# Optimization experiments

Hardware: AMD Instinct MI355X
Metric: run time of the kernel (lower is better)

## Reference

```python
import jax, jax.numpy as jnp
import numpy as np

N, E, D, H, O, L = 50000, 400000, 128, 128, 64, 2


def setup_inputs() -> dict:
    key = jax.random.key(0)
    ks = jax.random.split(key, 24)
    s = 0.05
    rn = lambda k, shape: jax.random.normal(k, shape, jnp.float32) * s
    # random edges with no self-loops (dst = src + nonzero offset mod N)
    src = jax.random.randint(ks[0], (E,), 0, N, dtype=jnp.int32)
    off = jax.random.randint(ks[1], (E,), 1, N, dtype=jnp.int32)
    dst = (src + off) % N
    edge_index = jnp.stack([src, dst])  # [2, E] int32
    return {
        "x": rn(ks[2], (N, D)),
        "edge_index": edge_index,
        "attn_W": rn(ks[3], (L, 2 * D, 2)),
        "attn_b": rn(ks[4], (L, 2)),
        "mlp_W1": rn(ks[5], (L, D, H)),
        "mlp_b1": rn(ks[6], (L, H)),
        "mlp_W2": rn(ks[7], (L, H, H)),
        "mlp_b2": rn(ks[8], (L, H)),
        "bn_gamma": jnp.ones((L, H), jnp.float32),   # torch BatchNorm1d default affine init
        "bn_beta": jnp.zeros((L, H), jnp.float32),
        "gru_Wih": rn(ks[9], (D, 3 * H)),
        "gru_Whh": rn(ks[10], (H, 3 * H)),
        "gru_bih": rn(ks[11], (3 * H,)),
        "gru_bhh": rn(ks[12], (3 * H,)),
        "last_W1": rn(ks[13], (H, H)),
        "last_b1": rn(ks[14], (H,)),
        "last_W2": rn(ks[15], (H, O)),
        "last_b2": rn(ks[16], (O,)),
    }


def reference(x, edge_index, attn_W, attn_b, mlp_W1, mlp_b1, mlp_W2, mlp_b2,
              bn_gamma, bn_beta, gru_Wih, gru_Whh, gru_bih, gru_bhh,
              last_W1, last_b1, last_W2, last_b2):
    n = x.shape[0]
    # symmetrize edge list: message (nbr -> node) for both directions
    node = jnp.concatenate([edge_index[0], edge_index[1]])  # destination
    nbr = jnp.concatenate([edge_index[1], edge_index[0]])   # source / neighbor
    deg = jax.ops.segment_sum(jnp.ones((node.shape[0], 1), x.dtype), node, num_segments=n)
    has_nbr = deg > 0

    h_state = jnp.zeros((n, gru_Whh.shape[0]), x.dtype)
    for l in range(attn_W.shape[0]):
        feats = x[nbr]  # [2E, d] gather
        s_agg = jax.ops.segment_sum(feats, node, num_segments=n)
        m_agg = jax.ops.segment_max(feats, node, num_segments=n)
        m_agg = jnp.where(has_nbr, m_agg, jnp.zeros_like(m_agg))  # isolated nodes stay 0
        # attention over {sum, max} aggregations
        scores = jnp.concatenate([s_agg, m_agg], axis=1) @ attn_W[l] + attn_b[l]  # [n, 2]
        w = jax.nn.softmax(scores, axis=1)
        comb = x + w[:, :1] * s_agg + w[:, 1:] * m_agg
        # MLP (in -> hidden, ReLU, hidden -> out)
        z = jax.nn.relu(comb @ mlp_W1[l] + mlp_b1[l]) @ mlp_W2[l] + mlp_b2[l]
        # BatchNorm1d in eval mode with running stats (mean 0, var 1): affine only
        z = z * bn_gamma[l] + bn_beta[l]
        # GRUCell
        gi = z @ gru_Wih + gru_bih
        gh = h_state @ gru_Whh + gru_bhh
        ir, iz, inn = jnp.split(gi, 3, axis=1)
        hr, hz, hn = jnp.split(gh, 3, axis=1)
        r = jax.nn.sigmoid(ir + hr)
        u = jax.nn.sigmoid(iz + hz)
        ncand = jnp.tanh(inn + r * hn)
        h_state = (1.0 - u) * ncand + u * h_state
        x = h_state
    # final node-level MLP
    out = jax.nn.relu(x @ last_W1 + last_b1) @ last_W2 + last_b2
    return out
```

## Files before the change

### kernel.cpp

```cpp
#include <hip/hip_runtime.h>
#include <math.h>

typedef unsigned short u16;
typedef __attribute__((ext_vector_type(8))) short bf16x8;
typedef __attribute__((ext_vector_type(4))) float f32x4;

#define ADJ_CAP 96

__device__ __forceinline__ u16 f2b(float f) {
    union { float f; unsigned u; } v; v.f = f;
    unsigned r = (v.u + 0x7FFF + ((v.u >> 16) & 1)) >> 16;
    return (u16)r;
}
__device__ __forceinline__ float b2f(u16 h) {
    union { unsigned u; float f; } v; v.u = (unsigned)h << 16;
    return v.f;
}
__device__ __forceinline__ float fsig(float x) { return 1.f / (1.f + __expf(-x)); }
__device__ __forceinline__ float ftanh(float x) {
    float e = __expf(2.f * x);
    return 1.f - 2.f / (e + 1.f);
}

__device__ __forceinline__ void gll16(const void* g, void* l) {
    __builtin_amdgcn_global_load_lds(
        (const __attribute__((address_space(1))) void*)g,
        (__attribute__((address_space(3))) void*)l, 16, 0, 0);
}

__device__ __forceinline__ void conv_chunk(const float* __restrict__ src,
                                           u16* __restrict__ dst, int c, int NC) {
    int sl = c / NC, n = c - sl * NC;
    u16 tmp[8];
#pragma unroll
    for (int i = 0; i < 8; ++i) tmp[i] = f2b(src[(size_t)(sl * 8 + i) * NC + n]);
    *(uint4*)(dst + (size_t)c * 8) = *(const uint4*)tmp;
}

__global__ void k_pro(const int* __restrict__ ei, int* __restrict__ cnt,
                      u16* __restrict__ adj, int E, int N,
                      const float* __restrict__ W1, const float* __restrict__ W2,
                      const float* __restrict__ Wih, const float* __restrict__ Whh,
                      const float* __restrict__ lW1, const float* __restrict__ lW2,
                      u16* __restrict__ tW1, u16* __restrict__ tW2,
                      u16* __restrict__ tGRU,
                      u16* __restrict__ tlW1, u16* __restrict__ tlW2, int L,
                      const float* __restrict__ x, u16* __restrict__ xb, int n8) {
    const int EB = (E + 255) >> 8;
    const int nwc = L * 4096 + 12288 + 3072;
    const int WB = (nwc + 255) >> 8;
    int b = blockIdx.x;
    if (b < EB * 8) {
        const int part = b & 7, chunk = b >> 3;
        const int span = (N + 7) >> 3;
        const int nlo = part * span;
        const int nhi = (nlo + span < N) ? nlo + span : N;
        int e = chunk * 256 + threadIdx.x;
        if (e < E) {
            int s = ei[e], d = ei[E + e];
            if (s >= nlo && s < nhi) {
                int p = atomicAdd(&cnt[s], 1);
                adj[(size_t)s * ADJ_CAP + p] = (u16)d;
            }
            if (d >= nlo && d < nhi) {
                int q = atomicAdd(&cnt[d], 1);
                adj[(size_t)d * ADJ_CAP + q] = (u16)s;
            }
        }
        return;
    }
    b -= EB * 8;
    if (b < WB) {
        int c = b * 256 + threadIdx.x;
        if (c >= nwc) return;
        if (c < L * 2048) { int l = c >> 11; conv_chunk(W1 + (size_t)l * 16384, tW1 + (size_t)l * 16384, c & 2047, 128); return; }
        c -= L * 2048;
        if (c < L * 2048) { int l = c >> 11; conv_chunk(W2 + (size_t)l * 16384, tW2 + (size_t)l * 16384, c & 2047, 128); return; }
        c -= L * 2048;
        if (c < 12288) {
            int s = c >> 9, r = c & 511;
            int q = r >> 7, mat = (r >> 6) & 1, cc = r & 63;
            int h = s / 12, s2 = s % 12, kc = s2 / 3, g = s2 % 3;
            int ocol = g * 128 + h * 64 + cc;
            const float* src = mat ? Whh : Wih;
            int kb = (kc * 4 + q) * 8;
            u16 tmp[8];
#pragma unroll
            for (int e = 0; e < 8; ++e) tmp[e] = f2b(src[(size_t)(kb + e) * 384 + ocol]);
            *(uint4*)(tGRU + (size_t)c * 8) = *(const uint4*)tmp;
            return;
        }
        c -= 12288;
        if (c < 2048) { conv_chunk(lW1, tlW1, c, 128); return; }
        c -= 2048;
        if (c < 1024) { conv_chunk(lW2, tlW2, c, 64); return; }
        return;
    }
    b -= WB;
    {
        int i = b * 256 + threadIdx.x;
        if (i < n8) {
            float4 a = *(const float4*)(x + (size_t)i * 8);
            float4 bb = *(const float4*)(x + (size_t)i * 8 + 4);
            u16 t[8] = {f2b(a.x), f2b(a.y), f2b(a.z), f2b(a.w),
                        f2b(bb.x), f2b(bb.y), f2b(bb.z), f2b(bb.w)};
            *(uint4*)(xb + (size_t)i * 8) = *(const uint4*)t;
        }
    }
}

__global__ __launch_bounds__(256) void k_agg(const u16* __restrict__ xb,
                                             const u16* __restrict__ adj,
                                             const int* __restrict__ cnt,
                                             const float* __restrict__ aW,
                                             const float* __restrict__ ab,
                                             u16* __restrict__ comb, int N) {
    int n = blockIdx.x * 4 + (threadIdx.x >> 6);
    if (n >= N) return;
    int l = threadIdx.x & 63;
    int half = l >> 5, e0 = (l & 31) * 4;
    int beg = n * ADJ_CAP;
    int deg = cnt[n];
    int end = beg + deg;
    float s0 = 0.f, s1 = 0.f, s2 = 0.f, s3 = 0.f;
    float m0 = -3.402823e38f, m1 = m0, m2 = m0, m3 = m0;
    int j = beg + half;
    for (; j + 14 < end; j += 16) {
        ushort4 v[8];
#pragma unroll
        for (int u = 0; u < 8; ++u) {
            int a = adj[j + 2 * u];
            v[u] = *(const ushort4*)(xb + (size_t)a * 128 + e0);
        }
#pragma unroll
        for (int u = 0; u < 8; ++u) {
            float f0 = b2f(v[u].x), f1 = b2f(v[u].y), f2 = b2f(v[u].z), f3 = b2f(v[u].w);
            s0 += f0; s1 += f1; s2 += f2; s3 += f3;
            m0 = fmaxf(m0, f0); m1 = fmaxf(m1, f1);
            m2 = fmaxf(m2, f2); m3 = fmaxf(m3, f3);
        }
    }
    for (; j < end; j += 2) {
        int nb = adj[j];
        ushort4 v = *(const ushort4*)(xb + (size_t)nb * 128 + e0);
        float f0 = b2f(v.x), f1 = b2f(v.y), f2 = b2f(v.z), f3 = b2f(v.w);
        s0 += f0; s1 += f1; s2 += f2; s3 += f3;
        m0 = fmaxf(m0, f0); m1 = fmaxf(m1, f1); m2 = fmaxf(m2, f2); m3 = fmaxf(m3, f3);
    }
    s0 += __shfl_xor(s0, 32); m0 = fmaxf(m0, __shfl_xor(m0, 32));
    s1 += __shfl_xor(s1, 32); m1 = fmaxf(m1, __shfl_xor(m1, 32));
    s2 += __shfl_xor(s2, 32); m2 = fmaxf(m2, __shfl_xor(m2, 32));
    s3 += __shfl_xor(s3, 32); m3 = fmaxf(m3, __shfl_xor(m3, 32));
    if (deg == 0) { m0 = m1 = m2 = m3 = 0.f; }
    float p0 = 0.f, p1 = 0.f;
    {
        float2 w0v = *(const float2*)(aW + (size_t)e0 * 2);
        float2 w1v = *(const float2*)(aW + (size_t)(e0 + 1) * 2);
        float2 w2v = *(const float2*)(aW + (size_t)(e0 + 2) * 2);
        float2 w3v = *(const float2*)(aW + (size_t)(e0 + 3) * 2);
        float2 u0v = *(const float2*)(aW + (size_t)(128 + e0) * 2);
        float2 u1v = *(const float2*)(aW + (size_t)(128 + e0 + 1) * 2);
        float2 u2v = *(const float2*)(aW + (size_t)(128 + e0 + 2) * 2);
        float2 u3v = *(const float2*)(aW + (size_t)(128 + e0 + 3) * 2);
        p0 = s0 * w0v.x + s1 * w1v.x + s2 * w2v.x + s3 * w3v.x
           + m0 * u0v.x + m1 * u1v.x + m2 * u2v.x + m3 * u3v.x;
        p1 = s0 * w0v.y + s1 * w1v.y + s2 * w2v.y + s3 * w3v.y
           + m0 * u0v.y + m1 * u1v.y + m2 * u2v.y + m3 * u3v.y;
    }
#pragma unroll
    for (int o = 16; o; o >>= 1) { p0 += __shfl_xor(p0, o); p1 += __shfl_xor(p1, o); }
    p0 += ab[0]; p1 += ab[1];
    float pm = fmaxf(p0, p1);
    float ea = __expf(p0 - pm), eb = __expf(p1 - pm);
    float w0 = ea / (ea + eb), w1 = 1.f - w0;
    if (half == 0) {
        ushort4 xv = *(const ushort4*)(xb + (size_t)n * 128 + e0);
        ushort4 o;
        o.x = f2b(b2f(xv.x) + w0 * s0 + w1 * m0);
        o.y = f2b(b2f(xv.y) + w0 * s1 + w1 * m1);
        o.z = f2b(b2f(xv.z) + w0 * s2 + w1 * m2);
        o.w = f2b(b2f(xv.w) + w0 * s3 + w1 * m3);
        *(ushort4*)(comb + (size_t)n * 128 + e0) = o;
    }
}

template <bool H0, bool WF32>
__global__ __launch_bounds__(256, 4) void k_layer(
    const u16* __restrict__ Cb, const u16* __restrict__ Hb,
    const float* __restrict__ Hf,
    const u16* __restrict__ W1t, const float* __restrict__ b1,
    const u16* __restrict__ W2t, const float* __restrict__ b2,
    const float* __restrict__ gam, const float* __restrict__ bet,
    const u16* __restrict__ tG,
    const float* __restrict__ bih, const float* __restrict__ bhh,
    float* __restrict__ HnF, u16* __restrict__ HnB, int M) {
    __shared__ __align__(16) u16 x_s[64 * 16 * 8];
    __shared__ __align__(16) u16 b_s[3][4096];
    const int t = threadIdx.x;
    const int m0 = blockIdx.x * 64;
    const int wid = t >> 6, lane = t & 63, lo = lane & 15, hi = lane >> 4;
    const int arow = 16 * wid + lo;

    auto issue = [&](int s) {
        const u16* g = (s < 4) ? (W1t + (size_t)s * 4096)
                     : (s < 8) ? (W2t + (size_t)(s - 4) * 4096)
                               : (tG + (size_t)(s - 8) * 4096);
        char* l = (char*)b_s[s % 3] + wid * 2048;
        const char* gp = (const char*)g + wid * 2048 + lane * 16;
        gll16(gp, l);
        gll16(gp + 1024, l + 1024);
    };

    float b1r[8], g2r[8], t2r[8];
#pragma unroll
    for (int j = 0; j < 8; ++j) {
        int c = 16 * j + lo;
        b1r[j] = b1[c];
        float gv = gam[c];
        g2r[j] = gv;
        t2r[j] = b2[c] * gv + bet[c];
    }
#pragma unroll
    for (int i = 0; i < 4; ++i) {
        int off = (i * 4 + wid) * 1024;
        int row = (off >> 8) + (lane >> 4);
        int sl = lane & 15;
        int gr = m0 + row; gr = gr < M ? gr : M - 1;
        gll16(Cb + (size_t)gr * 128 + ((sl ^ (row & 7)) * 8), (char*)x_s + off);
    }
    issue(0);
    issue(1);

    f32x4 acc[8];
#pragma unroll
    for (int j = 0; j < 8; ++j) acc[j] = (f32x4)0.f;

#pragma unroll
    for (int ks = 0; ks < 4; ++ks) {
        const int p = ks;
        asm volatile("s_waitcnt vmcnt(2)" ::: "memory");
        __builtin_amdgcn_s_barrier();
        issue(p + 2);
        bf16x8 af = *(const bf16x8*)&x_s[(arow * 16 + ((ks * 4 + hi) ^ (arow & 7))) * 8];
        const u16* buf = b_s[p % 3];
        __builtin_amdgcn_s_setprio(1);
#pragma unroll
        for (int j = 0; j < 8; ++j) {
            bf16x8 bf = *(const bf16x8*)&buf[((size_t)hi * 128 + 16 * j + lo) * 8];
            acc[j] = __builtin_amdgcn_mfma_f32_16x16x32_bf16(af, bf, acc[j], 0, 0, 0);
        }
        __builtin_amdgcn_s_setprio(0);
    }
#pragma unroll
    for (int j = 0; j < 8; ++j) {
        int c = 16 * j + lo;
#pragma unroll
        for (int q = 0; q < 4; ++q) {
            int row = 16 * wid + hi * 4 + q;
            float v = fmaxf(acc[j][q] + b1r[j], 0.f);
            int sl = c >> 3;
            x_s[(row * 16 + (sl ^ (row & 7))) * 8 + (c & 7)] = f2b(v);
        }
        acc[j] = (f32x4)0.f;
    }

#pragma unroll
    for (int ks = 0; ks < 4; ++ks) {
        const int p = 4 + ks;
        asm volatile("s_waitcnt vmcnt(2)" ::: "memory");
        __builtin_amdgcn_s_barrier();
        issue(p + 2);
        bf16x8 af = *(const bf16x8*)&x_s[(arow * 16 + ((ks * 4 + hi) ^ (arow & 7))) * 8];
        const u16* buf = b_s[p % 3];
        __builtin_amdgcn_s_setprio(1);
#pragma unroll
        for (int j = 0; j < 8; ++j) {
            bf16x8 bf = *(const bf16x8*)&buf[((size_t)hi * 128 + 16 * j + lo) * 8];
            acc[j] = __builtin_amdgcn_mfma_f32_16x16x32_bf16(af, bf, acc[j], 0, 0, 0);
        }
        __builtin_amdgcn_s_setprio(0);
    }
#pragma unroll
    for (int j = 0; j < 8; ++j) {
        int c = 16 * j + lo;
#pragma unroll
        for (int q = 0; q < 4; ++q) {
            int row = 16 * wid + hi * 4 + q;
            float v = acc[j][q] * g2r[j] + t2r[j];
            int sl = c >> 3;
            x_s[(row * 16 + (sl ^ (row & 7))) * 8 + (c & 7)] = f2b(v);
        }
    }
    bf16x8 hreg[4];
    if (!H0) {
        int gr = m0 + arow; gr = gr < M ? gr : M - 1;
#pragma unroll
        for (int kc = 0; kc < 4; ++kc)
            hreg[kc] = *(const bf16x8*)(Hb + (size_t)gr * 128 + (kc * 4 + hi) * 8);
    }

    f32x4 racc[4], uacc[4], nza[4], nha[4];

    auto epi = [&](int h) {
#pragma unroll
        for (int ct = 0; ct < 4; ++ct) {
            int c = h * 64 + ct * 16 + lo;
            float b_r = bih[c] + bhh[c];
            float b_u = bih[c + 128] + bhh[c + 128];
            float b_in = bih[c + 256], b_hn = bhh[c + 256];
#pragma unroll
            for (int q = 0; q < 4; ++q) {
                int r = m0 + 16 * wid + hi * 4 + q;
                if (r < M) {
                    float rr = fsig(racc[ct][q] + b_r);
                    float uu = fsig(uacc[ct][q] + b_u);
                    float hterm = H0 ? b_hn : (nha[ct][q] + b_hn);
                    float nn = ftanh(nza[ct][q] + b_in + rr * hterm);
                    float hv = H0 ? 0.f : Hf[(size_t)r * 128 + c];
                    float o = (1.f - uu) * nn + uu * hv;
                    if (WF32) HnF[(size_t)r * 128 + c] = o;
                    HnB[(size_t)r * 128 + c] = f2b(o);
                }
            }
        }
    };

#pragma unroll
    for (int h = 0; h < 2; ++h) {
#pragma unroll
        for (int j = 0; j < 4; ++j) {
            racc[j] = (f32x4)0.f; uacc[j] = (f32x4)0.f;
            nza[j] = (f32x4)0.f; nha[j] = (f32x4)0.f;
        }
#pragma unroll
        for (int kc = 0; kc < 4; ++kc) {
            bf16x8 zf;
#pragma unroll
            for (int g = 0; g < 3; ++g) {
                const int p = 8 + h * 12 + kc * 3 + g;
                if (p == 31) asm volatile("s_waitcnt vmcnt(0)" ::: "memory");
                else         asm volatile("s_waitcnt vmcnt(2)" ::: "memory");
                __builtin_amdgcn_s_barrier();
                if (p + 2 <= 31) issue(p + 2);
                if (g == 0)
                    zf = *(const bf16x8*)&x_s[(arow * 16 + ((kc * 4 + hi) ^ (arow & 7))) * 8];
                const u16* buf = b_s[p % 3];
                __builtin_amdgcn_s_setprio(1);
#pragma unroll
                for (int jj = 0; jj < 4; ++jj) {
                    bf16x8 wi = *(const bf16x8*)&buf[((size_t)hi * 128 + jj * 16 + lo) * 8];
                    if (g == 0)      racc[jj] = __builtin_amdgcn_mfma_f32_16x16x32_bf16(zf, wi, racc[jj], 0, 0, 0);
                    else if (g == 1) uacc[jj] = __builtin_amdgcn_mfma_f32_16x16x32_bf16(zf, wi, uacc[jj], 0, 0, 0);
                    else             nza[jj]  = __builtin_amdgcn_mfma_f32_16x16x32_bf16(zf, wi, nza[jj], 0, 0, 0);
                    if (!H0) {
                        bf16x8 wh = *(const bf16x8*)&buf[((size_t)hi * 128 + 64 + jj * 16 + lo) * 8];
                        if (g == 0)      racc[jj] = __builtin_amdgcn_mfma_f32_16x16x32_bf16(hreg[kc], wh, racc[jj], 0, 0, 0);
                        else if (g == 1) uacc[jj] = __builtin_amdgcn_mfma_f32_16x16x32_bf16(hreg[kc], wh, uacc[jj], 0, 0, 0);
                        else             nha[jj]  = __builtin_amdgcn_mfma_f32_16x16x32_bf16(hreg[kc], wh, nha[jj], 0, 0, 0);
                    }
                }
                __builtin_amdgcn_s_setprio(0);
            }
        }
        epi(h);
    }
}

__global__ __launch_bounds__(256, 2) void k_final(const u16* __restrict__ Hb,
                                                  const u16* __restrict__ W1t,
                                                  const float* __restrict__ b1,
                                                  const u16* __restrict__ W2t,
                                                  const float* __restrict__ b2,
                                                  float* __restrict__ out, int M) {
    __shared__ __align__(16) u16 x_s[64 * 16 * 8];
    __shared__ __align__(16) u16 w_s[16 * 128 * 8];
    const int t = threadIdx.x;
    const int m0 = blockIdx.x * 64;
    const int w = t >> 6, l = t & 63, lo = l & 15, hi = l >> 4;
    const int arow = 16 * w + lo;
#pragma unroll
    for (int i = 0; i < 4; ++i) {
        int idx = t + i * 256;
        int row = idx >> 4, sl = idx & 15;
        int gr = m0 + row; gr = gr < M ? gr : M - 1;
        *(uint4*)&x_s[(row * 16 + (sl ^ (row & 7))) * 8] =
            *(const uint4*)(Hb + (size_t)gr * 128 + sl * 8);
    }
#pragma unroll
    for (int i = 0; i < 8; ++i) {
        int idx = t + i * 256;
        *(uint4*)&w_s[idx * 8] = *(const uint4*)(W1t + (size_t)idx * 8);
    }
    __syncthreads();
    f32x4 acc[8];
#pragma unroll
    for (int j = 0; j < 8; ++j) acc[j] = (f32x4)0.f;
#pragma unroll
    for (int ks = 0; ks < 4; ++ks) {
        bf16x8 af = *(const bf16x8*)&x_s[(arow * 16 + ((ks * 4 + hi) ^ (arow & 7))) * 8];
#pragma unroll
        for (int j = 0; j < 8; ++j) {
            bf16x8 bf = *(const bf16x8*)&w_s[((ks * 4 + hi) * 128 + 16 * j + lo) * 8];
            acc[j] = __builtin_amdgcn_mfma_f32_16x16x32_bf16(af, bf, acc[j], 0, 0, 0);
        }
    }
    __syncthreads();
#pragma unroll
    for (int j = 0; j < 8; ++j) {
        int c = 16 * j + lo;
        float bv = b1[c];
#pragma unroll
        for (int q = 0; q < 4; ++q) {
            int row = 16 * w + hi * 4 + q;
            float v = fmaxf(acc[j][q] + bv, 0.f);
            int sl = c >> 3;
            x_s[(row * 16 + (sl ^ (row & 7))) * 8 + (c & 7)] = f2b(v);
        }
    }
#pragma unroll
    for (int i = 0; i < 4; ++i) {
        int idx = t + i * 256;
        *(uint4*)&w_s[idx * 8] = *(const uint4*)(W2t + (size_t)idx * 8);
    }
    __syncthreads();
    f32x4 a2[4];
#pragma unroll
    for (int j = 0; j < 4; ++j) a2[j] = (f32x4)0.f;
#pragma unroll
    for (int ks = 0; ks < 4; ++ks) {
        bf16x8 af = *(const bf16x8*)&x_s[(arow * 16 + ((ks * 4 + hi) ^ (arow & 7))) * 8];
#pragma unroll
        for (int j = 0; j < 4; ++j) {
            bf16x8 bf = *(const bf16x8*)&w_s[((ks * 4 + hi) * 64 + 16 * j + lo) * 8];
            a2[j] = __builtin_amdgcn_mfma_f32_16x16x32_bf16(af, bf, a2[j], 0, 0, 0);
        }
    }
#pragma unroll
    for (int j = 0; j < 4; ++j) {
        int c = 16 * j + lo;
        float bv = b2[c];
#pragma unroll
        for (int q = 0; q < 4; ++q) {
            int r = m0 + 16 * w + hi * 4 + q;
            if (r < M) out[(size_t)r * 64 + c] = a2[j][q] + bv;
        }
    }
}

extern "C" void kernel_launch(void* const* d_in, const int* in_sizes, int n_in,
                              void* d_out, int out_size, void* d_ws, size_t ws_size,
                              hipStream_t stream) {
    const float* x   = (const float*)d_in[0];
    const int*   ei  = (const int*)d_in[1];
    const float* aW  = (const float*)d_in[2];
    const float* ab  = (const float*)d_in[3];
    const float* W1  = (const float*)d_in[4];
    const float* b1  = (const float*)d_in[5];
    const float* W2  = (const float*)d_in[6];
    const float* b2  = (const float*)d_in[7];
    const float* gam = (const float*)d_in[8];
    const float* bet = (const float*)d_in[9];
    const float* Wih = (const float*)d_in[10];
    const float* Whh = (const float*)d_in[11];
    const float* bih = (const float*)d_in[12];
    const float* bhh = (const float*)d_in[13];
    const float* lW1 = (const float*)d_in[14];
    const float* lb1 = (const float*)d_in[15];
    const float* lW2 = (const float*)d_in[16];
    const float* lb2 = (const float*)d_in[17];

    const int N = in_sizes[0] / 128;
    const int E = in_sizes[1] / 2;
    const int L = in_sizes[3] / 2;
    float* out = (float*)d_out;

    char* ws = (char*)d_ws;
    size_t off = 0;
    auto alloc = [&](size_t bytes) -> void* {
        void* p = ws + off;
        off = (off + bytes + 255) & ~(size_t)255;
        return p;
    };
    int* cnt  = (int*)alloc((size_t)N * 4);
    u16* adj  = (u16*)alloc((size_t)N * ADJ_CAP * 2);
    u16* tW1  = (u16*)alloc((size_t)L * 16384 * 2);
    u16* tW2  = (u16*)alloc((size_t)L * 16384 * 2);
    u16* tGRU = (u16*)alloc((size_t)98304 * 2);
    u16* tlW1 = (u16*)alloc((size_t)16384 * 2);
    u16* tlW2 = (u16*)alloc((size_t)8192 * 2);
    u16* xb   = (u16*)alloc((size_t)N * 128 * 2);
    u16* comb = (u16*)alloc((size_t)N * 128 * 2);
    float* hF = (float*)alloc((size_t)N * 128 * 4);
    u16* hAb  = (u16*)alloc((size_t)N * 128 * 2);
    u16* hBb  = (u16*)alloc((size_t)N * 128 * 2);
    (void)ws_size; (void)n_in; (void)out_size;

    hipMemsetAsync(cnt, 0, (size_t)N * 4, stream);

    const int EB = (E + 255) / 256;
    const int nwc = L * 4096 + 12288 + 3072;
    const int WB = (nwc + 255) / 256;
    const int FB = (N * 16 + 255) / 256;
    k_pro<<<EB * 8 + WB + FB, 256, 0, stream>>>(ei, cnt, adj, E, N,
                                                W1, W2, Wih, Whh, lW1, lW2,
                                                tW1, tW2, tGRU, tlW1, tlW2, L,
                                                x, xb, N * 16);

    const int mb = (N + 63) / 64;
    k_agg<<<(N + 3) / 4, 256, 0, stream>>>(xb, adj, cnt, aW, ab, comb, N);
    k_layer<true, true><<<mb, 256, 0, stream>>>(
        comb, nullptr, nullptr, tW1, b1, tW2, b2, gam, bet,
        tGRU, bih, bhh, hF, hAb, N);
    k_agg<<<(N + 3) / 4, 256, 0, stream>>>(hAb, adj, cnt, aW + 512, ab + 2, comb, N);
    k_layer<false, false><<<mb, 256, 0, stream>>>(
        comb, hAb, hF, tW1 + 16384, b1 + 128, tW2 + 16384, b2 + 128,
        gam + 128, bet + 128, tGRU, bih, bhh, nullptr, hBb, N);

    k_final<<<(N + 63) / 64, 256, 0, stream>>>(hBb, tlW1, lb1, tlW2, lb2, out, N);
}
```

Before: 222.4 us.

## Fuse final MLP into last GRU layer, drop fp32 hidden state, widen agg loads

```diff
diff --git a/kernel.cpp b/kernel.cpp
--- a/kernel.cpp
+++ b/kernel.cpp
@@ -14,6 +14,10 @@
 }
 __device__ __forceinline__ float b2f(u16 h) {
     union { unsigned u; float f; } v; v.u = (unsigned)h << 16;
+    return v.f;
+}
+__device__ __forceinline__ float u2f(unsigned u) {
+    union { unsigned u; float f; } v; v.u = u;
     return v.f;
 }
 __device__ __forceinline__ float fsig(float x) { return 1.f / (1.f + __expf(-x)); }
@@ -118,93 +122,105 @@
     int n = blockIdx.x * 4 + (threadIdx.x >> 6);
     if (n >= N) return;
     int l = threadIdx.x & 63;
-    int half = l >> 5, e0 = (l & 31) * 4;
-    int beg = n * ADJ_CAP;
-    int deg = cnt[n];
-    int end = beg + deg;
-    float s0 = 0.f, s1 = 0.f, s2 = 0.f, s3 = 0.f;
-    float m0 = -3.402823e38f, m1 = m0, m2 = m0, m3 = m0;
-    int j = beg + half;
-    for (; j + 14 < end; j += 16) {
-        ushort4 v[8];
-#pragma unroll
-        for (int u = 0; u < 8; ++u) {
-            int a = adj[j + 2 * u];
-            v[u] = *(const ushort4*)(xb + (size_t)a * 128 + e0);
-        }
-#pragma unroll
-        for (int u = 0; u < 8; ++u) {
-            float f0 = b2f(v[u].x), f1 = b2f(v[u].y), f2 = b2f(v[u].z), f3 = b2f(v[u].w);
-            s0 += f0; s1 += f1; s2 += f2; s3 += f3;
-            m0 = fmaxf(m0, f0); m1 = fmaxf(m1, f1);
-            m2 = fmaxf(m2, f2); m3 = fmaxf(m3, f3);
-        }
-    }
-    for (; j < end; j += 2) {
-        int nb = adj[j];
-        ushort4 v = *(const ushort4*)(xb + (size_t)nb * 128 + e0);
-        float f0 = b2f(v.x), f1 = b2f(v.y), f2 = b2f(v.z), f3 = b2f(v.w);
-        s0 += f0; s1 += f1; s2 += f2; s3 += f3;
-        m0 = fmaxf(m0, f0); m1 = fmaxf(m1, f1); m2 = fmaxf(m2, f2); m3 = fmaxf(m3, f3);
-    }
-    s0 += __shfl_xor(s0, 32); m0 = fmaxf(m0, __shfl_xor(m0, 32));
-    s1 += __shfl_xor(s1, 32); m1 = fmaxf(m1, __shfl_xor(m1, 32));
-    s2 += __shfl_xor(s2, 32); m2 = fmaxf(m2, __shfl_xor(m2, 32));
-    s3 += __shfl_xor(s3, 32); m3 = fmaxf(m3, __shfl_xor(m3, 32));
-    if (deg == 0) { m0 = m1 = m2 = m3 = 0.f; }
+    int grp = l >> 4;
+    int f0 = (l & 15) * 8;
+    int beg = n * ADJ_CAP, deg = cnt[n], end = beg + deg;
+    float s[8], m[8];
+#pragma unroll
+    for (int i = 0; i < 8; ++i) { s[i] = 0.f; m[i] = -3.402823e38f; }
+
+    auto acc8 = [&](uint4 v) {
+        unsigned d[4] = {v.x, v.y, v.z, v.w};
+#pragma unroll
+        for (int i = 0; i < 4; ++i) {
+            float a0 = u2f(d[i] << 16);
+            float a1 = u2f(d[i] & 0xFFFF0000u);
+            s[2 * i] += a0;     m[2 * i] = fmaxf(m[2 * i], a0);
+            s[2 * i + 1] += a1; m[2 * i + 1] = fmaxf(m[2 * i + 1], a1);
+        }
+    };
+
+    int j = beg + grp;
+    for (; j + 4 < end; j += 8) {
+        int a0 = adj[j], a1 = adj[j + 4];
+        uint4 v0 = *(const uint4*)(xb + (size_t)a0 * 128 + f0);
+        uint4 v1 = *(const uint4*)(xb + (size_t)a1 * 128 + f0);
+        acc8(v0);
+        acc8(v1);
+    }
+    if (j < end) {
+        int a = adj[j];
+        uint4 v = *(const uint4*)(xb + (size_t)a * 128 + f0);
+        acc8(v);
+    }
+#pragma unroll
+    for (int i = 0; i < 8; ++i) {
+        s[i] += __shfl_xor(s[i], 16);
+        s[i] += __shfl_xor(s[i], 32);
+        m[i] = fmaxf(m[i], __shfl_xor(m[i], 16));
+        m[i] = fmaxf(m[i], __shfl_xor(m[i], 32));
+    }
+    if (deg == 0) {
+#pragma unroll
+        for (int i = 0; i < 8; ++i) m[i] = 0.f;
+    }
     float p0 = 0.f, p1 = 0.f;
-    {
-        float2 w0v = *(const float2*)(aW + (size_t)e0 * 2);
-        float2 w1v = *(const float2*)(aW + (size_t)(e0 + 1) * 2);
-        float2 w2v = *(const float2*)(aW + (size_t)(e0 + 2) * 2);
-        float2 w3v = *(const float2*)(aW + (size_t)(e0 + 3) * 2);
-        float2 u0v = *(const float2*)(aW + (size_t)(128 + e0) * 2);
-        float2 u1v = *(const float2*)(aW + (size_t)(128 + e0 + 1) * 2);
-        float2 u2v = *(const float2*)(aW + (size_t)(128 + e0 + 2) * 2);
-        float2 u3v = *(const float2*)(aW + (size_t)(128 + e0 + 3) * 2);
-        p0 = s0 * w0v.x + s1 * w1v.x + s2 * w2v.x + s3 * w3v.x
-           + m0 * u0v.x + m1 * u1v.x + m2 * u2v.x + m3 * u3v.x;
-        p1 = s0 * w0v.y + s1 * w1v.y + s2 * w2v.y + s3 * w3v.y
-           + m0 * u0v.y + m1 * u1v.y + m2 * u2v.y + m3 * u3v.y;
-    }
-#pragma unroll
-    for (int o = 16; o; o >>= 1) { p0 += __shfl_xor(p0, o); p1 += __shfl_xor(p1, o); }
+#pragma unroll
+    for (int i = 0; i < 8; ++i) {
+        float2 wS = *(const float2*)(aW + (size_t)(f0 + i) * 2);
+        float2 wM = *(const float2*)(aW + (size_t)(128 + f0 + i) * 2);
+        p0 += s[i] * wS.x + m[i] * wM.x;
+        p1 += s[i] * wS.y + m[i] * wM.y;
+    }
+#pragma unroll
+    for (int o = 8; o; o >>= 1) { p0 += __shfl_xor(p0, o); p1 += __shfl_xor(p1, o); }
     p0 += ab[0]; p1 += ab[1];
     float pm = fmaxf(p0, p1);
     float ea = __expf(p0 - pm), eb = __expf(p1 - pm);
     float w0 = ea / (ea + eb), w1 = 1.f - w0;
-    if (half == 0) {
-        ushort4 xv = *(const ushort4*)(xb + (size_t)n * 128 + e0);
-        ushort4 o;
-        o.x = f2b(b2f(xv.x) + w0 * s0 + w1 * m0);
-        o.y = f2b(b2f(xv.y) + w0 * s1 + w1 * m1);
-        o.z = f2b(b2f(xv.z) + w0 * s2 + w1 * m2);
-        o.w = f2b(b2f(xv.w) + w0 * s3 + w1 * m3);
-        *(ushort4*)(comb + (size_t)n * 128 + e0) = o;
-    }
-}
-
-template <bool H0, bool WF32>
+    if (grp == 0) {
+        uint4 xv = *(const uint4*)(xb + (size_t)n * 128 + f0);
+        unsigned xs[4] = {xv.x, xv.y, xv.z, xv.w};
+        unsigned dw[4];
+#pragma unroll
+        for (int i = 0; i < 4; ++i) {
+            float xlo = u2f(xs[i] << 16), xhi = u2f(xs[i] & 0xFFFF0000u);
+            float olo = xlo + w0 * s[2 * i] + w1 * m[2 * i];
+            float ohi = xhi + w0 * s[2 * i + 1] + w1 * m[2 * i + 1];
+            dw[i] = (unsigned)f2b(olo) | ((unsigned)f2b(ohi) << 16);
+        }
+        uint4 o4 = make_uint4(dw[0], dw[1], dw[2], dw[3]);
+        *(uint4*)(comb + (size_t)n * 128 + f0) = o4;
+    }
+}
+
+template <bool H0, bool FIN>
 __global__ __launch_bounds__(256, 4) void k_layer(
     const u16* __restrict__ Cb, const u16* __restrict__ Hb,
-    const float* __restrict__ Hf,
     const u16* __restrict__ W1t, const float* __restrict__ b1,
     const u16* __restrict__ W2t, const float* __restrict__ b2,
     const float* __restrict__ gam, const float* __restrict__ bet,
     const u16* __restrict__ tG,
     const float* __restrict__ bih, const float* __restrict__ bhh,
-    float* __restrict__ HnF, u16* __restrict__ HnB, int M) {
+    u16* __restrict__ HnB,
+    const u16* __restrict__ lW1t, const float* __restrict__ lb1,
+    const u16* __restrict__ lW2t, const float* __restrict__ lb2,
+    float* __restrict__ out, int M) {
     __shared__ __align__(16) u16 x_s[64 * 16 * 8];
     __shared__ __align__(16) u16 b_s[3][4096];
     const int t = threadIdx.x;
     const int m0 = blockIdx.x * 64;
     const int wid = t >> 6, lane = t & 63, lo = lane & 15, hi = lane >> 4;
     const int arow = 16 * wid + lo;
+    const int LAST = FIN ? 37 : 31;
 
     auto issue = [&](int s) {
-        const u16* g = (s < 4) ? (W1t + (size_t)s * 4096)
-                     : (s < 8) ? (W2t + (size_t)(s - 4) * 4096)
-                               : (tG + (size_t)(s - 8) * 4096);
+        const u16* g;
+        if (s < 4)                 g = W1t + (size_t)s * 4096;
+        else if (s < 8)            g = W2t + (size_t)(s - 4) * 4096;
+        else if (!FIN || s < 32)   g = tG + (size_t)(s - 8) * 4096;
+        else if (s < 36)           g = lW1t + (size_t)(s - 32) * 4096;
+        else                       g = lW2t + (size_t)(s - 36) * 4096;
         char* l = (char*)b_s[s % 3] + wid * 2048;
         const char* gp = (const char*)g + wid * 2048 + lane * 16;
         gll16(gp, l);
@@ -300,8 +316,9 @@
     }
 
     f32x4 racc[4], uacc[4], nza[4], nha[4];
-
-    auto epi = [&](int h) {
+    float o_all[2][4][4];
+
+    auto epi = [&](int h, float (&oo)[4][4]) {
 #pragma unroll
         for (int ct = 0; ct < 4; ++ct) {
             int c = h * 64 + ct * 16 + lo;
@@ -311,16 +328,17 @@
 #pragma unroll
             for (int q = 0; q < 4; ++q) {
                 int r = m0 + 16 * wid + hi * 4 + q;
+                float o = 0.f;
                 if (r < M) {
                     float rr = fsig(racc[ct][q] + b_r);
                     float uu = fsig(uacc[ct][q] + b_u);
                     float hterm = H0 ? b_hn : (nha[ct][q] + b_hn);
                     float nn = ftanh(nza[ct][q] + b_in + rr * hterm);
-                    float hv = H0 ? 0.f : Hf[(size_t)r * 128 + c];
-                    float o = (1.f - uu) * nn + uu * hv;
-                    if (WF32) HnF[(size_t)r * 128 + c] = o;
-                    HnB[(size_t)r * 128 + c] = f2b(o);
+                    float hv = H0 ? 0.f : b2f(Hb[(size_t)r * 128 + c]);
+                    o = (1.f - uu) * nn + uu * hv;
+                    if (!FIN) HnB[(size_t)r * 128 + c] = f2b(o);
                 }
+                if (FIN) oo[ct][q] = o;
             }
         }
     };
@@ -338,10 +356,10 @@
 #pragma unroll
             for (int g = 0; g < 3; ++g) {
                 const int p = 8 + h * 12 + kc * 3 + g;
-                if (p == 31) asm volatile("s_waitcnt vmcnt(0)" ::: "memory");
-                else         asm volatile("s_waitcnt vmcnt(2)" ::: "memory");
+                if (!FIN && p == 31) asm volatile("s_waitcnt vmcnt(0)" ::: "memory");
+                else                 asm volatile("s_waitcnt vmcnt(2)" ::: "memory");
                 __builtin_amdgcn_s_barrier();
-                if (p + 2 <= 31) issue(p + 2);
+                if (p + 2 <= LAST) issue(p + 2);
                 if (g == 0)
                     zf = *(const bf16x8*)&x_s[(arow * 16 + ((kc * 4 + hi) ^ (arow & 7))) * 8];
                 const u16* buf = b_s[p % 3];
@@ -362,87 +380,85 @@
                 __builtin_amdgcn_s_setprio(0);
             }
         }
-        epi(h);
-    }
-}
-
-__global__ __launch_bounds__(256, 2) void k_final(const u16* __restrict__ Hb,
-                                                  const u16* __restrict__ W1t,
-                                                  const float* __restrict__ b1,
-                                                  const u16* __restrict__ W2t,
-                                                  const float* __restrict__ b2,
-                                                  float* __restrict__ out, int M) {
-    __shared__ __align__(16) u16 x_s[64 * 16 * 8];
-    __shared__ __align__(16) u16 w_s[16 * 128 * 8];
-    const int t = threadIdx.x;
-    const int m0 = blockIdx.x * 64;
-    const int w = t >> 6, l = t & 63, lo = l & 15, hi = l >> 4;
-    const int arow = 16 * w + lo;
-#pragma unroll
-    for (int i = 0; i < 4; ++i) {
-        int idx = t + i * 256;
-        int row = idx >> 4, sl = idx & 15;
-        int gr = m0 + row; gr = gr < M ? gr : M - 1;
-        *(uint4*)&x_s[(row * 16 + (sl ^ (row & 7))) * 8] =
-            *(const uint4*)(Hb + (size_t)gr * 128 + sl * 8);
-    }
-#pragma unroll
-    for (int i = 0; i < 8; ++i) {
-        int idx = t + i * 256;
-        *(uint4*)&w_s[idx * 8] = *(const uint4*)(W1t + (size_t)idx * 8);
-    }
-    __syncthreads();
-    f32x4 acc[8];
-#pragma unroll
-    for (int j = 0; j < 8; ++j) acc[j] = (f32x4)0.f;
-#pragma unroll
-    for (int ks = 0; ks < 4; ++ks) {
-        bf16x8 af = *(const bf16x8*)&x_s[(arow * 16 + ((ks * 4 + hi) ^ (arow & 7))) * 8];
+        epi(h, o_all[h]);
+    }
+
+    if (FIN) {
+#pragma unroll
+        for (int h = 0; h < 2; ++h)
+#pragma unroll
+            for (int ct = 0; ct < 4; ++ct) {
+                int c = h * 64 + ct * 16 + lo;
+#pragma unroll
+                for (int q = 0; q < 4; ++q) {
+                    int row = 16 * wid + hi * 4 + q;
+                    int sl = c >> 3;
+                    x_s[(row * 16 + (sl ^ (row & 7))) * 8 + (c & 7)] = f2b(o_all[h][ct][q]);
+                }
+            }
+#pragma unroll
+        for (int j = 0; j < 8; ++j) acc[j] = (f32x4)0.f;
+#pragma unroll
+        for (int ks = 0; ks < 4; ++ks) {
+            const int p = 32 + ks;
+            asm volatile("s_waitcnt vmcnt(2)" ::: "memory");
+            __builtin_amdgcn_s_barrier();
+            if (p + 2 <= 37) issue(p + 2);
+            bf16x8 af = *(const bf16x8*)&x_s[(arow * 16 + ((ks * 4 + hi) ^ (arow & 7))) * 8];
+            const u16* buf = b_s[p % 3];
+            __builtin_amdgcn_s_setprio(1);
+#pragma unroll
+            for (int j = 0; j < 8; ++j) {
+                bf16x8 bf = *(const bf16x8*)&buf[((size_t)hi * 128 + 16 * j + lo) * 8];
+                acc[j] = __builtin_amdgcn_mfma_f32_16x16x32_bf16(af, bf, acc[j], 0, 0, 0);
+            }
+            __builtin_amdgcn_s_setprio(0);
+        }
 #pragma unroll
         for (int j = 0; j < 8; ++j) {
-            bf16x8 bf = *(const bf16x8*)&w_s[((ks * 4 + hi) * 128 + 16 * j + lo) * 8];
-            acc[j] = __builtin_amdgcn_mfma_f32_16x16x32_bf16(af, bf, acc[j], 0, 0, 0);
-        }
-    }
-    __syncthreads();
-#pragma unroll
-    for (int j = 0; j < 8; ++j) {
-        int c = 16 * j + lo;
-        float bv = b1[c];
-#pragma unroll
-        for (int q = 0; q < 4; ++q) {
-            int row = 16 * w + hi * 4 + q;
-            float v = fmaxf(acc[j][q] + bv, 0.f);
-            int sl = c >> 3;
-            x_s[(row * 16 + (sl ^ (row & 7))) * 8 + (c & 7)] = f2b(v);
-        }
-    }
-#pragma unroll
-    for (int i = 0; i < 4; ++i) {
-        int idx = t + i * 256;
-        *(uint4*)&w_s[idx * 8] = *(const uint4*)(W2t + (size_t)idx * 8);
-    }
-    __syncthreads();
-    f32x4 a2[4];
-#pragma unroll
-    for (int j = 0; j < 4; ++j) a2[j] = (f32x4)0.f;
-#pragma unroll
-    for (int ks = 0; ks < 4; ++ks) {
-        bf16x8 af = *(const bf16x8*)&x_s[(arow * 16 + ((ks * 4 + hi) ^ (arow & 7))) * 8];
-#pragma unroll
-        for (int j = 0; j < 4; ++j) {
-            bf16x8 bf = *(const bf16x8*)&w_s[((ks * 4 + hi) * 64 + 16 * j + lo) * 8];
-            a2[j] = __builtin_amdgcn_mfma_f32_16x16x32_bf16(af, bf, a2[j], 0, 0, 0);
-        }
-    }
-#pragma unroll
-    for (int j = 0; j < 4; ++j) {
-        int c = 16 * j + lo;
-        float bv = b2[c];
-#pragma unroll
-        for (int q = 0; q < 4; ++q) {
-            int r = m0 + 16 * w + hi * 4 + q;
-            if (r < M) out[(size_t)r * 64 + c] = a2[j][q] + bv;
+            int c = 16 * j + lo;
+            float bv = lb1[c];
+#pragma unroll
+            for (int q = 0; q < 4; ++q) {
+                int row = 16 * wid + hi * 4 + q;
+                float v = fmaxf(acc[j][q] + bv, 0.f);
+                int sl = c >> 3;
+                x_s[(row * 16 + (sl ^ (row & 7))) * 8 + (c & 7)] = f2b(v);
+            }
+        }
+        f32x4 a2[4];
+#pragma unroll
+        for (int j = 0; j < 4; ++j) a2[j] = (f32x4)0.f;
+#pragma unroll
+        for (int ph = 0; ph < 2; ++ph) {
+            const int p = 36 + ph;
+            if (p == 37) asm volatile("s_waitcnt vmcnt(0)" ::: "memory");
+            else         asm volatile("s_waitcnt vmcnt(2)" ::: "memory");
+            __builtin_amdgcn_s_barrier();
+            const u16* buf = b_s[p % 3];
+            __builtin_amdgcn_s_setprio(1);
+#pragma unroll
+            for (int k2 = 0; k2 < 2; ++k2) {
+                int ks = ph * 2 + k2;
+                bf16x8 af = *(const bf16x8*)&x_s[(arow * 16 + ((ks * 4 + hi) ^ (arow & 7))) * 8];
+                int lk = k2 * 4 + hi;
+#pragma unroll
+                for (int jj = 0; jj < 4; ++jj) {
+                    bf16x8 bf = *(const bf16x8*)&buf[((size_t)lk * 64 + 16 * jj + lo) * 8];
+                    a2[jj] = __builtin_amdgcn_mfma_f32_16x16x32_bf16(af, bf, a2[jj], 0, 0, 0);
+                }
+            }
+            __builtin_amdgcn_s_setprio(0);
+        }
+#pragma unroll
+        for (int jj = 0; jj < 4; ++jj) {
+            int c = 16 * jj + lo;
+            float bv = lb2[c];
+#pragma unroll
+            for (int q = 0; q < 4; ++q) {
+                int r = m0 + 16 * wid + hi * 4 + q;
+                if (r < M) out[(size_t)r * 64 + c] = a2[jj][q] + bv;
+            }
         }
     }
 }
@@ -490,9 +506,7 @@
     u16* tlW2 = (u16*)alloc((size_t)8192 * 2);
     u16* xb   = (u16*)alloc((size_t)N * 128 * 2);
     u16* comb = (u16*)alloc((size_t)N * 128 * 2);
-    float* hF = (float*)alloc((size_t)N * 128 * 4);
     u16* hAb  = (u16*)alloc((size_t)N * 128 * 2);
-    u16* hBb  = (u16*)alloc((size_t)N * 128 * 2);
     (void)ws_size; (void)n_in; (void)out_size;
 
     hipMemsetAsync(cnt, 0, (size_t)N * 4, stream);
@@ -508,13 +522,13 @@
 
     const int mb = (N + 63) / 64;
     k_agg<<<(N + 3) / 4, 256, 0, stream>>>(xb, adj, cnt, aW, ab, comb, N);
-    k_layer<true, true><<<mb, 256, 0, stream>>>(
-        comb, nullptr, nullptr, tW1, b1, tW2, b2, gam, bet,
-        tGRU, bih, bhh, hF, hAb, N);
+    k_layer<true, false><<<mb, 256, 0, stream>>>(
+        comb, nullptr, tW1, b1, tW2, b2, gam, bet,
+        tGRU, bih, bhh, hAb,
+        nullptr, nullptr, nullptr, nullptr, nullptr, N);
     k_agg<<<(N + 3) / 4, 256, 0, stream>>>(hAb, adj, cnt, aW + 512, ab + 2, comb, N);
-    k_layer<false, false><<<mb, 256, 0, stream>>>(
-        comb, hAb, hF, tW1 + 16384, b1 + 128, tW2 + 16384, b2 + 128,
-        gam + 128, bet + 128, tGRU, bih, bhh, nullptr, hBb, N);
-
-    k_final<<<(N + 63) / 64, 256, 0, stream>>>(hBb, tlW1, lb1, tlW2, lb2, out, N);
-}
+    k_layer<false, true><<<mb, 256, 0, stream>>>(
+        comb, hAb, tW1 + 16384, b1 + 128, tW2 + 16384, b2 + 128,
+        gam + 128, bet + 128, tGRU, bih, bhh, nullptr,
+        tlW1, lb1, tlW2, lb2, out, N);
+}
```

After: 245.0 us. 10.2% more time.
